# Kernel tuning notes

Hardware: AMD Instinct MI355X
Metric: run time of the kernel (lower is better)

Reference implementation:

```python
import jax, jax.numpy as jnp
import numpy as np

MAX_DIST = 10
FP_PENALTY = 2.0


def _min_dist_to(mask, BIG):
    """Per-position distance to the nearest True in mask along axis 1.

    mask: [B, S] bool. Returns int32 [B, S]; BIG where the row has no True.
    Replaces the O(B*S_switch^2) Python loops with two cummax scans.
    """
    B, S = mask.shape
    idx = jnp.arange(S, dtype=jnp.int32)
    def one_side(m):
        last = jax.lax.cummax(jnp.where(m, idx, jnp.int32(-BIG)), axis=1)
        return idx - last  # distance to nearest True at or before each position
    d_fwd = one_side(mask)
    d_bwd = jnp.flip(one_side(jnp.flip(mask, axis=1)), axis=1)
    return jnp.minimum(jnp.minimum(d_fwd, d_bwd), BIG)


def setup_inputs() -> dict:
    key = jax.random.key(0)
    k1, k2 = jax.random.split(key)
    B, S, C = 256, 32768, 3
    logits = jax.random.normal(k1, (B, S, C), dtype=jnp.float32)
    labels = jax.random.randint(k2, (B, S), 0, 3, dtype=jnp.int32)
    distance_weights = jnp.array(
        [1.0, 0.99, 0.95, 0.9, 0.85, 0.8, 0.75, 0.7, 0.65, 0.6, 0.55], jnp.float32)
    class_weights = jnp.array([1.0, 10.0, 10.0], jnp.float32)
    return {"logits": logits, "labels": labels,
            "distance_weights": distance_weights, "class_weights": class_weights}


def reference(logits, labels, distance_weights, class_weights):
    B, S, C = logits.shape
    BIG = 2 * S

    valid = labels != -100
    safe_labels = jnp.where(valid, labels, 0)

    # weighted CE, reduction='none', ignore_index=-100
    logp = jax.nn.log_softmax(logits, axis=-1)
    nll = -jnp.take_along_axis(logp, safe_labels[..., None], axis=-1)[..., 0]
    ce = jnp.where(valid, nll * class_weights[safe_labels], 0.0)

    switch = (labels == 1) | (labels == 2)          # true switch positions
    preds = jnp.argmax(logits, axis=-1)
    pred_switch = (preds == 1) | (preds == 2)       # predicted switch positions

    d_to_true = _min_dist_to(switch, BIG)           # nearest true switch per position
    d_to_pred = _min_dist_to(pred_switch, BIG)      # nearest predicted switch per position

    validf = valid.astype(ce.dtype)

    # proximity bonus at valid predicted-switch positions near a true switch
    n_w = distance_weights.shape[0]
    w = jnp.take(distance_weights, jnp.clip(d_to_true, 0, n_w - 1))
    bonus_mask = pred_switch & valid & (d_to_true <= MAX_DIST)
    bonus = jnp.where(bonus_mask, ce * w * 0.5, 0.0)

    # double CE at valid true switches far from every predicted switch
    # (torch code skips this entirely when the row has no predicted switch)
    has_pred = jnp.any(pred_switch, axis=1, keepdims=True)
    double_mask = switch & valid & has_pred & (d_to_pred > MAX_DIST)
    ce = jnp.where(double_mask, ce * 2.0, ce) - bonus

    masked = ce * validf
    fp = pred_switch.astype(ce.dtype) * (1.0 - switch.astype(ce.dtype)) * validf * FP_PENALTY
    total = masked + fp
    return total.sum() / jnp.maximum(validf.sum(), 1.0)
```

## Files before the change

kernel.cpp:

```cpp
#include <hip/hip_runtime.h>
#include <stdint.h>

#define MAX_DIST 10
#define FP_PENALTY 2.0f
#define CHUNK 4096
#define NT 512
#define PPT (CHUNK / NT)
#define NG 2
#define GP 4
#define NBYTES (CHUNK / 8 + 4)
#define NDW ((NBYTES + 3) / 4)

typedef float f32x4 __attribute__((ext_vector_type(4)));
typedef int   i32x4 __attribute__((ext_vector_type(4)));

__global__ __launch_bounds__(NT, 8) void pal_main(
    const float* __restrict__ logits, const int* __restrict__ labels,
    const float* __restrict__ dw, const float* __restrict__ cw,
    double* __restrict__ blk_base, double* __restrict__ blk_extra,
    int* __restrict__ blk_valid, int* __restrict__ blk_haspred,
    int S, int chunks_per_row)
{
    __shared__ unsigned int swb32[NDW];
    __shared__ unsigned int psb32[NDW];
    __shared__ float tbl[12];
    __shared__ float rb[NT / 64], rex[NT / 64];
    __shared__ int rvfp[NT / 64], rp[NT / 64];

    unsigned char* swb = (unsigned char*)swb32;
    unsigned char* psb = (unsigned char*)psb32;

    const int t = threadIdx.x;
    const int wave = t >> 6, lane = t & 63;
    const int blk = blockIdx.x;
    const int row = blk / chunks_per_row;
    const int ck  = blk % chunks_per_row;
    const int s0  = ck * CHUNK;
    const long long rowbase = (long long)row * S;
    const long long pbase = rowbase + s0 + (long long)t * PPT;

    if (t < 12) tbl[t] = (t < 11) ? 0.5f * dw[t] : 0.0f;
    const float cw0 = cw[0], cw1 = cw[1], cw2 = cw[2];

    i32x4 lb0, lb1;
    f32x4 x00, x10, x20, x01, x11, x21;
    {
        const int*   la0 = labels + pbase;
        const int*   la1 = labels + pbase + GP;
        const float* lp0 = logits + pbase * 3;
        const float* lp1 = logits + (pbase + GP) * 3;
        asm volatile("global_load_dwordx4 %0, %1, off" : "=v"(lb0) : "v"(la0));
        asm volatile("global_load_dwordx4 %0, %1, off" : "=v"(x00) : "v"(lp0));
        asm volatile("global_load_dwordx4 %0, %1, off" : "=v"(x10) : "v"(lp0 + 4));
        asm volatile("global_load_dwordx4 %0, %1, off" : "=v"(x20) : "v"(lp0 + 8));
        asm volatile("global_load_dwordx4 %0, %1, off" : "=v"(lb1) : "v"(la1));
        asm volatile("global_load_dwordx4 %0, %1, off" : "=v"(x01) : "v"(lp1));
        asm volatile("global_load_dwordx4 %0, %1, off" : "=v"(x11) : "v"(lp1 + 4));
        asm volatile("global_load_dwordx4 %0, %1, off" : "=v"(x21) : "v"(lp1 + 8));
    }

    float ce[PPT];
    unsigned swm = 0u, psm = 0u, vvm = 0u;

#define PROCESS_GROUP(g, LB, X0, X1, X2)                                      \
    {                                                                         \
        const float L[12] = { X0.x, X0.y, X0.z, X0.w,                         \
                              X1.x, X1.y, X1.z, X1.w,                         \
                              X2.x, X2.y, X2.z, X2.w };                       \
        const int lbl4[4] = { LB.x, LB.y, LB.z, LB.w };                       \
        _Pragma("unroll")                                                     \
        for (int i = 0; i < GP; ++i) {                                        \
            const int j = (g) * GP + i;                                       \
            const int lbl = lbl4[i];                                          \
            const float l0 = L[3*i], l1 = L[3*i+1], l2 = L[3*i+2];            \
            int pred = 0; float best = l0;                                    \
            if (l1 > best) { best = l1; pred = 1; }                           \
            if (l2 > best) { best = l2; pred = 2; }                           \
            const bool valid = (lbl != -100);                                 \
            const int sl = valid ? lbl : 0;                                   \
            const float a = (pred == 0) ? l1 : l0;                            \
            const float b = (pred == 2) ? l1 : l2;                            \
            const float esum = 1.0f + __expf(a - best) + __expf(b - best);    \
            const float lse = best + __logf(esum);                            \
            const float lt  = (sl == 0) ? l0 : (sl == 1 ? l1 : l2);           \
            const float cwv = (sl == 0) ? cw0 : (sl == 1 ? cw1 : cw2);        \
            ce[j] = valid ? (lse - lt) * cwv : 0.0f;                          \
            swm |= ((lbl == 1) || (lbl == 2)) ? (1u << j) : 0u;               \
            psm |= (pred != 0) ? (1u << j) : 0u;                              \
            vvm |= valid ? (1u << j) : 0u;                                    \
        }                                                                     \
    }

    asm volatile("s_waitcnt vmcnt(4)" ::: "memory");
    __builtin_amdgcn_sched_barrier(0);
    PROCESS_GROUP(0, lb0, x00, x10, x20)
    asm volatile("s_waitcnt vmcnt(0)" ::: "memory");
    __builtin_amdgcn_sched_barrier(0);
    PROCESS_GROUP(1, lb1, x01, x11, x21)
#undef PROCESS_GROUP

    swb[t + 2] = (unsigned char)swm;
    psb[t + 2] = (unsigned char)psm;
    const int vfp = __popc(vvm) | (__popc(psm & ~swm & vvm) << 16);
    const bool anyp = (psm != 0u);

    if (wave == 0) {
        bool sw = false, ps = false;
        int s = -1;
        if (lane < 10) s = s0 - 10 + lane;
        else if (lane >= 32 && lane < 42) s = s0 + CHUNK + (lane - 32);
        if (s >= 0 && s < S) {
            const long long g = rowbase + s;
            const int lbl = labels[g];
            const float* lp = logits + g * 3;
            const float l0 = lp[0], l1 = lp[1], l2 = lp[2];
            int pred = 0; float best = l0;
            if (l1 > best) { best = l1; pred = 1; }
            if (l2 > best) { best = l2; pred = 2; }
            sw = (lbl == 1) || (lbl == 2);
            ps = (pred == 1) || (pred == 2);
        }
        const unsigned long long bs = __ballot(sw ? 1 : 0);
        const unsigned long long bp = __ballot(ps ? 1 : 0);
        if (lane == 0) {
            *(unsigned short*)&swb[0] = (unsigned short)((bs & 0x3FFull) << 6);
            *(unsigned short*)&psb[0] = (unsigned short)((bp & 0x3FFull) << 6);
            *(unsigned short*)&swb[CHUNK / 8 + 2] = (unsigned short)((bs >> 32) & 0x3FFull);
            *(unsigned short*)&psb[CHUNK / 8 + 2] = (unsigned short)((bp >> 32) & 0x3FFull);
        }
    }
    __syncthreads();

    const int di = t >> 2;
    const int off = ((t & 3) << 3) + 6;
    const unsigned sext = __builtin_amdgcn_alignbit(swb32[di + 1], swb32[di], off);
    const unsigned pext = __builtin_amdgcn_alignbit(psb32[di + 1], psb32[di], off);

    float base_acc = 0.0f, extra_acc = 0.0f;
    #pragma unroll
    for (int j = 0; j < PPT; ++j) {
        const unsigned swin = (sext >> j) & 0x1FFFFFu;
        const unsigned pwin = (pext >> j) & 0x1FFFFFu;

        const bool sw_self = (swin >> 10) & 1u;
        const bool ps_self = (pwin >> 10) & 1u;
        const bool npnear  = (pwin == 0u);

        const unsigned low10 = swin & 0x3FFu;
        const unsigned up10  = (swin >> 11) & 0x3FFu;
        const int ddown = __clz((low10 << 21) | 0x100000u);
        const int dup   = __ffs(up10 | 0x400u);
        int dt = min(ddown, dup);
        dt = sw_self ? 0 : dt;

        const float f = ps_self ? tbl[dt] : 0.0f;
        base_acc += ce[j] * (1.0f - f);
        extra_acc += (sw_self && npnear) ? ce[j] : 0.0f;
    }

    float ba = base_acc, ea = extra_acc; int vf = vfp;
    for (int offr = 32; offr; offr >>= 1) {
        ba += __shfl_down(ba, offr);
        ea += __shfl_down(ea, offr);
        vf += __shfl_down(vf, offr);
    }
    const bool wave_any = __any(anyp ? 1 : 0);
    if (lane == 0) {
        rb[wave] = ba; rex[wave] = ea; rvfp[wave] = vf; rp[wave] = wave_any ? 1 : 0;
    }
    __syncthreads();
    if (t == 0) {
        double bsum = 0.0, esum = 0.0; int vs = 0, fps = 0, ap = 0;
        for (int i = 0; i < NT / 64; ++i) {
            bsum += rb[i]; esum += rex[i];
            vs += rvfp[i] & 0xFFFF; fps += rvfp[i] >> 16; ap |= rp[i];
        }
        blk_base[blk]    = bsum + (double)FP_PENALTY * (double)fps;
        blk_extra[blk]   = esum;
        blk_valid[blk]   = vs;
        blk_haspred[blk] = ap;
    }
}

__global__ __launch_bounds__(256) void pal_finish(
    const double* __restrict__ blk_base, const double* __restrict__ blk_extra,
    const int* __restrict__ blk_valid, const int* __restrict__ blk_haspred,
    int nrows, int chunks_per_row, float* __restrict__ out)
{
    const int t = threadIdx.x;
    double bsum = 0.0, esum = 0.0;
    long long vsum = 0;
    for (int r = t; r < nrows; r += 256) {
        int hp = 0; double e = 0.0;
        for (int c = 0; c < chunks_per_row; ++c) {
            const int i = r * chunks_per_row + c;
            bsum += blk_base[i];
            e    += blk_extra[i];
            hp   |= blk_haspred[i];
            vsum += blk_valid[i];
        }
        if (hp) esum += e;
    }
    __shared__ double sb[256], se[256];
    __shared__ long long sv[256];
    sb[t] = bsum; se[t] = esum; sv[t] = vsum;
    __syncthreads();
    for (int off = 128; off; off >>= 1) {
        if (t < off) { sb[t] += sb[t + off]; se[t] += se[t + off]; sv[t] += sv[t + off]; }
        __syncthreads();
    }
    if (t == 0) {
        const double tot = sb[0] + se[0];
        double denom = (double)sv[0];
        if (denom < 1.0) denom = 1.0;
        out[0] = (float)(tot / denom);
    }
}

extern "C" void kernel_launch(void* const* d_in, const int* in_sizes, int n_in,
                              void* d_out, int out_size, void* d_ws, size_t ws_size,
                              hipStream_t stream)
{
    const float* logits = (const float*)d_in[0];
    const int*   labels = (const int*)d_in[1];
    const float* dw     = (const float*)d_in[2];
    const float* cw     = (const float*)d_in[3];

    const int S = 32768;
    const int Brows = in_sizes[1] / S;
    const int CPR = S / CHUNK;
    const int nblk = Brows * CPR;

    double* blk_base    = (double*)d_ws;
    double* blk_extra   = blk_base + nblk;
    int*    blk_valid   = (int*)(blk_extra + nblk);
    int*    blk_haspred = blk_valid + nblk;

    pal_main<<<nblk, NT, 0, stream>>>(logits, labels, dw, cw,
                                      blk_base, blk_extra, blk_valid, blk_haspred,
                                      S, CPR);
    pal_finish<<<1, 256, 0, stream>>>(blk_base, blk_extra, blk_valid, blk_haspred,
                                      Brows, CPR, (float*)d_out);
}
```

Before: 33.33 us.

## Double per-thread points to 16 and widen the halo bitmask to 16-bit words

New measurement: 39.93 us. +19.8%, slower.

```diff
diff --git a/kernel.cpp b/kernel.cpp
--- a/kernel.cpp
+++ b/kernel.cpp
@@ -3,18 +3,17 @@
 
 #define MAX_DIST 10
 #define FP_PENALTY 2.0f
-#define CHUNK 4096
 #define NT 512
-#define PPT (CHUNK / NT)
-#define NG 2
+#define PPT 16
+#define CHUNK (NT * PPT)
 #define GP 4
-#define NBYTES (CHUNK / 8 + 4)
-#define NDW ((NBYTES + 3) / 4)
+#define NSH (NT + 2)
+#define NDW ((NSH + 1) / 2)
 
 typedef float f32x4 __attribute__((ext_vector_type(4)));
 typedef int   i32x4 __attribute__((ext_vector_type(4)));
 
-__global__ __launch_bounds__(NT, 8) void pal_main(
+__global__ __launch_bounds__(NT, 4) void pal_main(
     const float* __restrict__ logits, const int* __restrict__ labels,
     const float* __restrict__ dw, const float* __restrict__ cw,
     double* __restrict__ blk_base, double* __restrict__ blk_extra,
@@ -27,8 +26,8 @@
     __shared__ float rb[NT / 64], rex[NT / 64];
     __shared__ int rvfp[NT / 64], rp[NT / 64];
 
-    unsigned char* swb = (unsigned char*)swb32;
-    unsigned char* psb = (unsigned char*)psb32;
+    unsigned short* swb = (unsigned short*)swb32;
+    unsigned short* psb = (unsigned short*)psb32;
 
     const int t = threadIdx.x;
     const int wave = t >> 6, lane = t & 63;
@@ -42,21 +41,27 @@
     if (t < 12) tbl[t] = (t < 11) ? 0.5f * dw[t] : 0.0f;
     const float cw0 = cw[0], cw1 = cw[1], cw2 = cw[2];
 
-    i32x4 lb0, lb1;
-    f32x4 x00, x10, x20, x01, x11, x21;
+    i32x4 lb0, lb1, lb2, lb3;
+    f32x4 x00, x10, x20, x01, x11, x21, x02, x12, x22, x03, x13, x23;
     {
-        const int*   la0 = labels + pbase;
-        const int*   la1 = labels + pbase + GP;
-        const float* lp0 = logits + pbase * 3;
-        const float* lp1 = logits + (pbase + GP) * 3;
-        asm volatile("global_load_dwordx4 %0, %1, off" : "=v"(lb0) : "v"(la0));
-        asm volatile("global_load_dwordx4 %0, %1, off" : "=v"(x00) : "v"(lp0));
-        asm volatile("global_load_dwordx4 %0, %1, off" : "=v"(x10) : "v"(lp0 + 4));
-        asm volatile("global_load_dwordx4 %0, %1, off" : "=v"(x20) : "v"(lp0 + 8));
-        asm volatile("global_load_dwordx4 %0, %1, off" : "=v"(lb1) : "v"(la1));
-        asm volatile("global_load_dwordx4 %0, %1, off" : "=v"(x01) : "v"(lp1));
-        asm volatile("global_load_dwordx4 %0, %1, off" : "=v"(x11) : "v"(lp1 + 4));
-        asm volatile("global_load_dwordx4 %0, %1, off" : "=v"(x21) : "v"(lp1 + 8));
+        const int* la = labels + pbase;
+        const float* lp = logits + pbase * 3;
+        asm volatile("global_load_dwordx4 %0, %1, off" : "=v"(lb0) : "v"(la));
+        asm volatile("global_load_dwordx4 %0, %1, off" : "=v"(x00) : "v"(lp));
+        asm volatile("global_load_dwordx4 %0, %1, off" : "=v"(x10) : "v"(lp + 4));
+        asm volatile("global_load_dwordx4 %0, %1, off" : "=v"(x20) : "v"(lp + 8));
+        asm volatile("global_load_dwordx4 %0, %1, off" : "=v"(lb1) : "v"(la + GP));
+        asm volatile("global_load_dwordx4 %0, %1, off" : "=v"(x01) : "v"(lp + 12));
+        asm volatile("global_load_dwordx4 %0, %1, off" : "=v"(x11) : "v"(lp + 16));
+        asm volatile("global_load_dwordx4 %0, %1, off" : "=v"(x21) : "v"(lp + 20));
+        asm volatile("global_load_dwordx4 %0, %1, off" : "=v"(lb2) : "v"(la + 2 * GP));
+        asm volatile("global_load_dwordx4 %0, %1, off" : "=v"(x02) : "v"(lp + 24));
+        asm volatile("global_load_dwordx4 %0, %1, off" : "=v"(x12) : "v"(lp + 28));
+        asm volatile("global_load_dwordx4 %0, %1, off" : "=v"(x22) : "v"(lp + 32));
+        asm volatile("global_load_dwordx4 %0, %1, off" : "=v"(lb3) : "v"(la + 3 * GP));
+        asm volatile("global_load_dwordx4 %0, %1, off" : "=v"(x03) : "v"(lp + 36));
+        asm volatile("global_load_dwordx4 %0, %1, off" : "=v"(x13) : "v"(lp + 40));
+        asm volatile("global_load_dwordx4 %0, %1, off" : "=v"(x23) : "v"(lp + 44));
     }
 
     float ce[PPT];
@@ -91,16 +96,22 @@
         }                                                                     \
     }
 
+    asm volatile("s_waitcnt vmcnt(12)" ::: "memory");
+    __builtin_amdgcn_sched_barrier(0);
+    PROCESS_GROUP(0, lb0, x00, x10, x20)
+    asm volatile("s_waitcnt vmcnt(8)" ::: "memory");
+    __builtin_amdgcn_sched_barrier(0);
+    PROCESS_GROUP(1, lb1, x01, x11, x21)
     asm volatile("s_waitcnt vmcnt(4)" ::: "memory");
     __builtin_amdgcn_sched_barrier(0);
-    PROCESS_GROUP(0, lb0, x00, x10, x20)
+    PROCESS_GROUP(2, lb2, x02, x12, x22)
     asm volatile("s_waitcnt vmcnt(0)" ::: "memory");
     __builtin_amdgcn_sched_barrier(0);
-    PROCESS_GROUP(1, lb1, x01, x11, x21)
+    PROCESS_GROUP(3, lb3, x03, x13, x23)
 #undef PROCESS_GROUP
 
-    swb[t + 2] = (unsigned char)swm;
-    psb[t + 2] = (unsigned char)psm;
+    swb[t + 1] = (unsigned short)swm;
+    psb[t + 1] = (unsigned short)psm;
     const int vfp = __popc(vvm) | (__popc(psm & ~swm & vvm) << 16);
     const bool anyp = (psm != 0u);
 
@@ -123,24 +134,27 @@
         const unsigned long long bs = __ballot(sw ? 1 : 0);
         const unsigned long long bp = __ballot(ps ? 1 : 0);
         if (lane == 0) {
-            *(unsigned short*)&swb[0] = (unsigned short)((bs & 0x3FFull) << 6);
-            *(unsigned short*)&psb[0] = (unsigned short)((bp & 0x3FFull) << 6);
-            *(unsigned short*)&swb[CHUNK / 8 + 2] = (unsigned short)((bs >> 32) & 0x3FFull);
-            *(unsigned short*)&psb[CHUNK / 8 + 2] = (unsigned short)((bp >> 32) & 0x3FFull);
+            swb[0] = (unsigned short)((bs & 0x3FFull) << 6);
+            psb[0] = (unsigned short)((bp & 0x3FFull) << 6);
+            swb[NT + 1] = (unsigned short)((bs >> 32) & 0x3FFull);
+            psb[NT + 1] = (unsigned short)((bp >> 32) & 0x3FFull);
         }
     }
     __syncthreads();
 
-    const int di = t >> 2;
-    const int off = ((t & 3) << 3) + 6;
-    const unsigned sext = __builtin_amdgcn_alignbit(swb32[di + 1], swb32[di], off);
-    const unsigned pext = __builtin_amdgcn_alignbit(psb32[di + 1], psb32[di], off);
+    const int bit0 = 16 * t + 6;
+    const int di = bit0 >> 5;
+    const int sh = bit0 & 31;
+    const unsigned sd0 = swb32[di], sd1 = swb32[di + 1];
+    const unsigned pd0 = psb32[di], pd1 = psb32[di + 1];
+    const unsigned slo = __builtin_amdgcn_alignbit(sd1, sd0, sh), shi_ = sd1 >> sh;
+    const unsigned plo = __builtin_amdgcn_alignbit(pd1, pd0, sh), phi_ = pd1 >> sh;
 
     float base_acc = 0.0f, extra_acc = 0.0f;
     #pragma unroll
     for (int j = 0; j < PPT; ++j) {
-        const unsigned swin = (sext >> j) & 0x1FFFFFu;
-        const unsigned pwin = (pext >> j) & 0x1FFFFFu;
+        const unsigned swin = __builtin_amdgcn_alignbit(shi_, slo, j) & 0x1FFFFFu;
+        const unsigned pwin = __builtin_amdgcn_alignbit(phi_, plo, j) & 0x1FFFFFu;
 
         const bool sw_self = (swin >> 10) & 1u;
         const bool ps_self = (pwin >> 10) & 1u;
```
